# Performance work log

Hardware: AMD Instinct MI355X
Metric: run time of the kernel (lower is better)

## Reference

```python
import jax, jax.numpy as jnp
import numpy as np

H, W = 480, 640
CLAMP = -1.0


def setup_inputs() -> dict:
    key = jax.random.key(0)
    ks = jax.random.split(key, 6)
    B = 16
    K = jnp.array([[500.0, 0.0, 320.0], [0.0, 500.0, 240.0], [0.0, 0.0, 1.0]], dtype=jnp.float32)
    Ki = jnp.linalg.inv(K)
    u, v = np.meshgrid(range(W), range(H))
    uv = np.stack((u, v, np.ones_like(u)), axis=2).reshape(-1, 3).astype(np.float32)
    ray = (jnp.asarray(uv) @ Ki.T).reshape(1, -1, 3).astype(jnp.float32)  # (1, H*W, 3)
    depth0 = jax.random.uniform(ks[0], (B, 1, H, W), jnp.float32)
    depth1 = jax.random.uniform(ks[1], (B, 1, H, W), jnp.float32)
    R0 = jax.random.normal(ks[2], (B, 3, 3), jnp.float32)
    t0 = jax.random.normal(ks[3], (B, 3), jnp.float32)
    R1 = jax.random.normal(ks[4], (B, 3, 3), jnp.float32)
    t1 = jax.random.normal(ks[5], (B, 3), jnp.float32)
    return {"depth0": depth0, "depth1": depth1, "R0": R0, "t0": t0, "R1": R1, "t1": t1, "K": K, "ray": ray}


def _grid_sample_border(img, gx, gy):
    # img: (B,H,W); gx,gy: (B,H,W) normalized coords in [-1,1].
    # Matches torch grid_sample(mode='bilinear', padding_mode='border', align_corners=False).
    B, h, w = img.shape
    x = jnp.clip(((gx + 1.0) * w - 1.0) * 0.5, 0.0, w - 1.0)
    y = jnp.clip(((gy + 1.0) * h - 1.0) * 0.5, 0.0, h - 1.0)
    x0 = jnp.floor(x)
    y0 = jnp.floor(y)
    wx = x - x0
    wy = y - y0
    x0i = x0.astype(jnp.int32)
    y0i = y0.astype(jnp.int32)
    x1i = jnp.minimum(x0i + 1, w - 1)
    y1i = jnp.minimum(y0i + 1, h - 1)
    b = jnp.arange(B)[:, None, None]
    v00 = img[b, y0i, x0i]
    v01 = img[b, y0i, x1i]
    v10 = img[b, y1i, x0i]
    v11 = img[b, y1i, x1i]
    return (1.0 - wy) * ((1.0 - wx) * v00 + wx * v01) + wy * ((1.0 - wx) * v10 + wx * v11)


def _fwd_one(depth0, depth1, R0, t0, R1, t1, K, ray):
    B = depth0.shape[0]
    xyz = depth0.reshape(B, -1, 1) * ray                        # unproject: (B,N,3)
    xyz = jnp.einsum('bnk,bkj->bnj', xyz - t0[:, None, :], R0)  # transform into world
    xyz = jnp.einsum('bnk,bjk->bnj', xyz, R1) + t1[:, None, :]  # project: xyz @ R1^T + t1
    uvd = jnp.einsum('bnk,jk->bnj', xyz, K)                     # xyz @ K^T
    d = uvd[..., 2]
    denom = jax.nn.relu(d) + 1e-12
    gx = 2.0 * (uvd[..., 0] / denom / (W - 1) - 0.5)
    gy = 2.0 * (uvd[..., 1] / denom / (H - 1) - 0.5)
    sampled = _grid_sample_border(depth1[:, 0], gx.reshape(B, H, W), gy.reshape(B, H, W))
    diff = jnp.abs(d.reshape(-1) - sampled.reshape(-1))
    if CLAMP > 0:
        diff = jnp.clip(diff, 0.0, CLAMP)
    return diff.mean()


def reference(depth0, depth1, R0, t0, R1, t1, K, ray):
    l0 = _fwd_one(depth0, depth1, R0, t0, R1, t1, K, ray)
    l1 = _fwd_one(depth1, depth0, R1, t1, R0, t0, K, ray)
    return l0 + l1
```

## Files before the change

### kernel.cpp

```cpp
#include <hip/hip_runtime.h>

#define HH 480
#define WW 640
#define NPIX (HH * WW)
#define BB 16
#define PPT 4
#define BLK 256
#define GX (NPIX / (BLK * PPT))
#define NPART (GX * BB * 2)

__global__ __launch_bounds__(BLK) void proj_depth_loss_kernel(
    const float* __restrict__ depth0, const float* __restrict__ depth1,
    const float* __restrict__ R0, const float* __restrict__ t0,
    const float* __restrict__ R1, const float* __restrict__ t1,
    const float* __restrict__ Km, const float* __restrict__ ray,
    float* __restrict__ ws)
{
    const int pass = blockIdx.z;
    const int b = blockIdx.y;
    const int n0 = (blockIdx.x * BLK + threadIdx.x) * PPT;

    const float* Ds = (pass == 0) ? depth0 : depth1;
    const float* Dt = (pass == 0) ? depth1 : depth0;
    const float* Ra = (pass == 0) ? R0 : R1;
    const float* ta = (pass == 0) ? t0 : t1;
    const float* Rb = (pass == 0) ? R1 : R0;
    const float* tb = (pass == 0) ? t1 : t0;

    const float* A = Ra + b * 9;
    const float* Bm = Rb + b * 9;
    float A0=A[0],A1=A[1],A2=A[2],A3=A[3],A4=A[4],A5=A[5],A6=A[6],A7=A[7],A8=A[8];
    float B0=Bm[0],B1=Bm[1],B2=Bm[2],B3=Bm[3],B4=Bm[4],B5=Bm[5],B6=Bm[6],B7=Bm[7],B8=Bm[8];
    float tax=ta[b*3+0], tay=ta[b*3+1], taz=ta[b*3+2];
    float tbx=tb[b*3+0], tby=tb[b*3+1], tbz=tb[b*3+2];
    float K0=Km[0],K1=Km[1],K2=Km[2],K3=Km[3],K4=Km[4],K5=Km[5],K6=Km[6],K7=Km[7],K8=Km[8];

    const float cw = (float)WW / (float)(WW - 1);
    const float ch = (float)HH / (float)(HH - 1);

    float4 d4 = *(const float4*)(Ds + b * NPIX + n0);
    const float4* rp = (const float4*)(ray + 3 * n0);
    float4 ra = rp[0], rbv = rp[1], rc = rp[2];

    float dd[PPT] = {d4.x, d4.y, d4.z, d4.w};
    float rx[PPT] = {ra.x, ra.w, rbv.z, rc.y};
    float ry[PPT] = {ra.y, rbv.x, rbv.w, rc.z};
    float rz[PPT] = {ra.z, rbv.y, rc.x, rc.w};

    float ud[PPT], wxf[PPT], wyf[PPT];
    int i00[PPT], i01[PPT], i10[PPT], i11[PPT];

    #pragma unroll
    for (int i = 0; i < PPT; ++i) {
        float d = dd[i];
        float x = d * rx[i] - tax;
        float y = d * ry[i] - tay;
        float z = d * rz[i] - taz;

        float wx = x * A0 + y * A3 + z * A6;
        float wy = x * A1 + y * A4 + z * A7;
        float wz = x * A2 + y * A5 + z * A8;

        float px = wx * B0 + wy * B1 + wz * B2 + tbx;
        float py = wx * B3 + wy * B4 + wz * B5 + tby;
        float pz = wx * B6 + wy * B7 + wz * B8 + tbz;

        float ux = K0 * px + K1 * py + K2 * pz;
        float uy = K3 * px + K4 * py + K5 * pz;
        float uu = K6 * px + K7 * py + K8 * pz;
        ud[i] = uu;

        float inv = 1.0f / (fmaxf(uu, 0.0f) + 1e-12f);
        float sx = ux * inv * cw - 0.5f;
        float sy = uy * inv * ch - 0.5f;
        sx = fminf(fmaxf(sx, 0.0f), (float)(WW - 1));
        sy = fminf(fmaxf(sy, 0.0f), (float)(HH - 1));
        float fx0 = floorf(sx);
        float fy0 = floorf(sy);
        wxf[i] = sx - fx0;
        wyf[i] = sy - fy0;
        int x0 = (int)fx0;
        int y0 = (int)fy0;
        int x1 = min(x0 + 1, WW - 1);
        int y1 = min(y0 + 1, HH - 1);
        i00[i] = y0 * WW + x0;
        i01[i] = y0 * WW + x1;
        i10[i] = y1 * WW + x0;
        i11[i] = y1 * WW + x1;
    }

    const float* img = Dt + b * NPIX;
    float v00[PPT], v01[PPT], v10[PPT], v11[PPT];
    #pragma unroll
    for (int i = 0; i < PPT; ++i) {
        v00[i] = img[i00[i]];
        v01[i] = img[i01[i]];
        v10[i] = img[i10[i]];
        v11[i] = img[i11[i]];
    }

    float diff = 0.0f;
    #pragma unroll
    for (int i = 0; i < PPT; ++i) {
        float s = (1.0f - wyf[i]) * ((1.0f - wxf[i]) * v00[i] + wxf[i] * v01[i])
                +         wyf[i]  * ((1.0f - wxf[i]) * v10[i] + wxf[i] * v11[i]);
        diff += fabsf(ud[i] - s);
    }

    for (int off = 32; off > 0; off >>= 1)
        diff += __shfl_down(diff, off, 64);

    __shared__ float partial[BLK / 64];
    const int wave = threadIdx.x >> 6;
    const int lane = threadIdx.x & 63;
    if (lane == 0) partial[wave] = diff;
    __syncthreads();
    if (threadIdx.x == 0) {
        float s = partial[0] + partial[1] + partial[2] + partial[3];
        ws[blockIdx.x + GX * (blockIdx.y + BB * blockIdx.z)] = s;
    }
}

__global__ __launch_bounds__(1024) void reduce_partials_kernel(
    const float* __restrict__ ws, float* __restrict__ out)
{
    float s = 0.0f;
    for (int i = threadIdx.x; i < NPART; i += 1024) s += ws[i];
    for (int off = 32; off > 0; off >>= 1)
        s += __shfl_down(s, off, 64);
    __shared__ float partial[16];
    const int wave = threadIdx.x >> 6;
    const int lane = threadIdx.x & 63;
    if (lane == 0) partial[wave] = s;
    __syncthreads();
    if (threadIdx.x == 0) {
        float tot = 0.0f;
        #pragma unroll
        for (int i = 0; i < 16; ++i) tot += partial[i];
        out[0] = tot * (1.0f / (float)((long long)BB * NPIX));
    }
}

extern "C" void kernel_launch(void* const* d_in, const int* in_sizes, int n_in,
                              void* d_out, int out_size, void* d_ws, size_t ws_size,
                              hipStream_t stream) {
    const float* depth0 = (const float*)d_in[0];
    const float* depth1 = (const float*)d_in[1];
    const float* R0     = (const float*)d_in[2];
    const float* t0     = (const float*)d_in[3];
    const float* R1     = (const float*)d_in[4];
    const float* t1     = (const float*)d_in[5];
    const float* Km     = (const float*)d_in[6];
    const float* ray    = (const float*)d_in[7];
    float* out = (float*)d_out;
    float* ws  = (float*)d_ws;

    dim3 block(BLK);
    dim3 grid(GX, BB, 2);
    proj_depth_loss_kernel<<<grid, block, 0, stream>>>(
        depth0, depth1, R0, t0, R1, t1, Km, ray, ws);
    reduce_partials_kernel<<<1, 1024, 0, stream>>>(ws, out);
}
```

Measured before the change: 121.5 us.

## Remap blocks per XCD, fold transforms into one matrix, double pixels per thread

```diff
diff --git a/kernel.cpp b/kernel.cpp
--- a/kernel.cpp
+++ b/kernel.cpp
@@ -4,10 +4,10 @@
 #define WW 640
 #define NPIX (HH * WW)
 #define BB 16
-#define PPT 4
+#define PPT 8
 #define BLK 256
-#define GX (NPIX / (BLK * PPT))
-#define NPART (GX * BB * 2)
+#define TILES (NPIX / (BLK * PPT))
+#define NPART (TILES * BB * 2)
 
 __global__ __launch_bounds__(BLK) void proj_depth_loss_kernel(
     const float* __restrict__ depth0, const float* __restrict__ depth1,
@@ -16,9 +16,14 @@
     const float* __restrict__ Km, const float* __restrict__ ray,
     float* __restrict__ ws)
 {
-    const int pass = blockIdx.z;
-    const int b = blockIdx.y;
-    const int n0 = (blockIdx.x * BLK + threadIdx.x) * PPT;
+    const int flat = blockIdx.x;
+    const int xcd = flat & 7;
+    const int j = flat >> 3;
+    const int pair_local = j / TILES;
+    const int tile = j - pair_local * TILES;
+    const int pair = xcd * 4 + pair_local;
+    const int pass = pair >> 4;
+    const int b = pair & 15;
 
     const float* Ds = (pass == 0) ? depth0 : depth1;
     const float* Dt = (pass == 0) ? depth1 : depth0;
@@ -29,50 +34,58 @@
 
     const float* A = Ra + b * 9;
     const float* Bm = Rb + b * 9;
-    float A0=A[0],A1=A[1],A2=A[2],A3=A[3],A4=A[4],A5=A[5],A6=A[6],A7=A[7],A8=A[8];
-    float B0=Bm[0],B1=Bm[1],B2=Bm[2],B3=Bm[3],B4=Bm[4],B5=Bm[5],B6=Bm[6],B7=Bm[7],B8=Bm[8];
+    float N_[9];
+    #pragma unroll
+    for (int i = 0; i < 3; ++i)
+        #pragma unroll
+        for (int jj = 0; jj < 3; ++jj)
+            N_[i*3+jj] = Bm[i*3+0]*A[jj*3+0] + Bm[i*3+1]*A[jj*3+1] + Bm[i*3+2]*A[jj*3+2];
     float tax=ta[b*3+0], tay=ta[b*3+1], taz=ta[b*3+2];
     float tbx=tb[b*3+0], tby=tb[b*3+1], tbz=tb[b*3+2];
-    float K0=Km[0],K1=Km[1],K2=Km[2],K3=Km[3],K4=Km[4],K5=Km[5],K6=Km[6],K7=Km[7],K8=Km[8];
+    float qx = tbx - (N_[0]*tax + N_[1]*tay + N_[2]*taz);
+    float qy = tby - (N_[3]*tax + N_[4]*tay + N_[5]*taz);
+    float qz = tbz - (N_[6]*tax + N_[7]*tay + N_[8]*taz);
+    float M_[9], cx, cy, cz;
+    #pragma unroll
+    for (int i = 0; i < 3; ++i)
+        #pragma unroll
+        for (int jj = 0; jj < 3; ++jj)
+            M_[i*3+jj] = Km[i*3+0]*N_[0*3+jj] + Km[i*3+1]*N_[1*3+jj] + Km[i*3+2]*N_[2*3+jj];
+    cx = Km[0]*qx + Km[1]*qy + Km[2]*qz;
+    cy = Km[3]*qx + Km[4]*qy + Km[5]*qz;
+    cz = Km[6]*qx + Km[7]*qy + Km[8]*qz;
 
-    const float cw = (float)WW / (float)(WW - 1);
-    const float ch = (float)HH / (float)(HH - 1);
+    const float cwf = (float)WW / (float)(WW - 1);
+    const float chf = (float)HH / (float)(HH - 1);
 
-    float4 d4 = *(const float4*)(Ds + b * NPIX + n0);
+    const int n0 = tile * (BLK * PPT) + threadIdx.x * PPT;
+
+    const float4* dp = (const float4*)(Ds + b * NPIX + n0);
+    float4 da = dp[0], db_ = dp[1];
     const float4* rp = (const float4*)(ray + 3 * n0);
-    float4 ra = rp[0], rbv = rp[1], rc = rp[2];
+    float4 r0 = rp[0], r1 = rp[1], r2 = rp[2], r3 = rp[3], r4 = rp[4], r5 = rp[5];
 
-    float dd[PPT] = {d4.x, d4.y, d4.z, d4.w};
-    float rx[PPT] = {ra.x, ra.w, rbv.z, rc.y};
-    float ry[PPT] = {ra.y, rbv.x, rbv.w, rc.z};
-    float rz[PPT] = {ra.z, rbv.y, rc.x, rc.w};
+    float dd[PPT] = {da.x, da.y, da.z, da.w, db_.x, db_.y, db_.z, db_.w};
+    float rx[PPT] = {r0.x, r0.w, r1.z, r2.y, r3.x, r3.w, r4.z, r5.y};
+    float ry[PPT] = {r0.y, r1.x, r1.w, r2.z, r3.y, r4.x, r4.w, r5.z};
+    float rz[PPT] = {r0.z, r1.y, r2.x, r2.w, r3.z, r4.y, r5.x, r5.w};
 
     float ud[PPT], wxf[PPT], wyf[PPT];
     int i00[PPT], i01[PPT], i10[PPT], i11[PPT];
 
     #pragma unroll
     for (int i = 0; i < PPT; ++i) {
-        float d = dd[i];
-        float x = d * rx[i] - tax;
-        float y = d * ry[i] - tay;
-        float z = d * rz[i] - taz;
-
-        float wx = x * A0 + y * A3 + z * A6;
-        float wy = x * A1 + y * A4 + z * A7;
-        float wz = x * A2 + y * A5 + z * A8;
-
-        float px = wx * B0 + wy * B1 + wz * B2 + tbx;
-        float py = wx * B3 + wy * B4 + wz * B5 + tby;
-        float pz = wx * B6 + wy * B7 + wz * B8 + tbz;
-
-        float ux = K0 * px + K1 * py + K2 * pz;
-        float uy = K3 * px + K4 * py + K5 * pz;
-        float uu = K6 * px + K7 * py + K8 * pz;
+        float mrx = M_[0]*rx[i] + M_[1]*ry[i] + M_[2]*rz[i];
+        float mry = M_[3]*rx[i] + M_[4]*ry[i] + M_[5]*rz[i];
+        float mrz = M_[6]*rx[i] + M_[7]*ry[i] + M_[8]*rz[i];
+        float ux = dd[i]*mrx + cx;
+        float uy = dd[i]*mry + cy;
+        float uu = dd[i]*mrz + cz;
         ud[i] = uu;
 
-        float inv = 1.0f / (fmaxf(uu, 0.0f) + 1e-12f);
-        float sx = ux * inv * cw - 0.5f;
-        float sy = uy * inv * ch - 0.5f;
+        float inv = __builtin_amdgcn_rcpf(fmaxf(uu, 0.0f) + 1e-12f);
+        float sx = ux * inv * cwf - 0.5f;
+        float sy = uy * inv * chf - 0.5f;
         sx = fminf(fmaxf(sx, 0.0f), (float)(WW - 1));
         sy = fminf(fmaxf(sy, 0.0f), (float)(HH - 1));
         float fx0 = floorf(sx);
@@ -102,8 +115,9 @@
     float diff = 0.0f;
     #pragma unroll
     for (int i = 0; i < PPT; ++i) {
-        float s = (1.0f - wyf[i]) * ((1.0f - wxf[i]) * v00[i] + wxf[i] * v01[i])
-                +         wyf[i]  * ((1.0f - wxf[i]) * v10[i] + wxf[i] * v11[i]);
+        float top = (1.0f - wxf[i]) * v00[i] + wxf[i] * v01[i];
+        float bot = (1.0f - wxf[i]) * v10[i] + wxf[i] * v11[i];
+        float s = (1.0f - wyf[i]) * top + wyf[i] * bot;
         diff += fabsf(ud[i] - s);
     }
 
@@ -117,7 +131,7 @@
     __syncthreads();
     if (threadIdx.x == 0) {
         float s = partial[0] + partial[1] + partial[2] + partial[3];
-        ws[blockIdx.x + GX * (blockIdx.y + BB * blockIdx.z)] = s;
+        ws[flat] = s;
     }
 }
 
@@ -155,9 +169,7 @@
     float* out = (float*)d_out;
     float* ws  = (float*)d_ws;
 
-    dim3 block(BLK);
-    dim3 grid(GX, BB, 2);
-    proj_depth_loss_kernel<<<grid, block, 0, stream>>>(
+    proj_depth_loss_kernel<<<dim3(NPART), dim3(BLK), 0, stream>>>(
         depth0, depth1, R0, t0, R1, t1, Km, ray, ws);
     reduce_partials_kernel<<<1, 1024, 0, stream>>>(ws, out);
 }
```

Measured after the change: 138.8 us. 1.14x slower.
